# Kernel tuning notes

Measured on AMD Instinct MI355X. Metric: run time of the kernel, lower is better.

## Reference

```python
import jax, jax.numpy as jnp
import numpy as np

N = 100000   # nodes
E = 3200000  # edges
F = 128      # input features
H = 6        # hiddenSize
C = 10       # num_classes
G = 512      # graphs in batch


def setup_inputs() -> dict:
    key = jax.random.key(0)
    ks = jax.random.split(key, 13)
    x = jax.random.normal(ks[0], (N, F), dtype=jnp.float32)
    edge_index = jax.random.randint(ks[1], (2, E), 0, N, dtype=jnp.int32)
    batch = jnp.sort(jax.random.randint(ks[2], (N,), 0, G, dtype=jnp.int32))

    def lin(k, fan_in, fan_out):
        return jax.random.normal(k, (fan_in, fan_out), dtype=jnp.float32) / np.sqrt(fan_in).astype(np.float32)

    return {
        "x": x, "edge_index": edge_index, "batch": batch,
        "W1": lin(ks[3], F, H), "b1": jnp.zeros((H,), jnp.float32),
        "W2": lin(ks[4], H, H), "b2": jnp.zeros((H,), jnp.float32),
        "W3": lin(ks[5], H, H), "b3": jnp.zeros((H,), jnp.float32),
        "W4": lin(ks[6], H, H), "b4": jnp.zeros((H,), jnp.float32),
        "Wf": lin(ks[7], H, C), "bf": jnp.zeros((C,), jnp.float32),
    }


def _gcn_conv(x, W, b, src, dst, norm):
    # x' = scatter_add_{dst}( norm * (x W)[src] ) + b   (GCNConv, sym-norm, self-loops)
    h = x @ W
    msg = norm[:, None] * h[src]
    return jax.ops.segment_sum(msg, dst, num_segments=N) + b


def reference(x, edge_index, batch, W1, b1, W2, b2, W3, b3, W4, b4, Wf, bf):
    loops = jnp.arange(N, dtype=edge_index.dtype)
    src = jnp.concatenate([edge_index[0], loops])
    dst = jnp.concatenate([edge_index[1], loops])
    # degree (with self-loops) at the aggregation side, symmetric normalization
    deg = jax.ops.segment_sum(jnp.ones_like(dst, dtype=jnp.float32), dst, num_segments=N)
    dinv = jnp.where(deg > 0, jax.lax.rsqrt(deg), 0.0)
    norm = dinv[src] * dinv[dst]

    h = jax.nn.relu(_gcn_conv(x, W1, b1, src, dst, norm))
    h = jax.nn.relu(_gcn_conv(h, W2, b2, src, dst, norm))
    h = jax.nn.relu(_gcn_conv(h, W3, b3, src, dst, norm))
    h = jax.nn.relu(_gcn_conv(h, W4, b4, src, dst, norm))
    h = jax.nn.relu(_gcn_conv(h, Wf, bf, src, dst, norm))  # [N, C]

    # global_mean_pool over graph ids
    sums = jax.ops.segment_sum(h, batch, num_segments=G)          # [G, C]
    counts = jax.ops.segment_sum(jnp.ones((N,), jnp.float32), batch, num_segments=G)
    pooled = sums / jnp.maximum(counts, 1.0)[:, None]
    return jax.nn.log_softmax(pooled, axis=1)
```

## Files before the change

### kernel.cpp

```cpp
#include <hip/hip_runtime.h>
#include <math.h>

#define NN 100000
#define EE 3200000
#define FF 128
#define HH 6
#define CC 10
#define GG 512
#define NBUCK 196
#define BCAP 20000
#define NSUB 4
#define SUBCAP 5000
#define PTILE 16384
#define SUBIT 5
#define GWIN 16

typedef _Float16 half8 __attribute__((ext_vector_type(8)));

__global__ __launch_bounds__(256) void k_setup(const int* __restrict__ batch,
                                               int* __restrict__ gcur,
                                               int* __restrict__ bounds,
                                               float* __restrict__ gpool) {
    int i = blockIdx.x * 256 + threadIdx.x;
    if (i < NBUCK * NSUB) gcur[i] = (i >> 2) * BCAP + (i & 3) * SUBCAP;
    if (i <= GG) {
        int lo = 0, hi = NN;
        while (lo < hi) {
            int mid = (lo + hi) >> 1;
            if (batch[mid] < i) lo = mid + 1; else hi = mid;
        }
        bounds[i] = lo;
    }
    for (int j = i; j < GG * CC; j += 1024) gpool[j] = 0.f;
}

__global__ __launch_bounds__(1024) void k_partition(const int* __restrict__ src,
                                                    const int* __restrict__ dst,
                                                    int* __restrict__ gcur,
                                                    int* __restrict__ part) {
    __shared__ int lcnt[NBUCK], lbase[NBUCK];
    int t = threadIdx.x;
    int slot = blockIdx.x & (NSUB - 1);
    if (t < NBUCK) lcnt[t] = 0;
    __syncthreads();
    int base = blockIdx.x * PTILE;
    int d[16], s[16], r[16];
#pragma unroll
    for (int k = 0; k < 16; ++k) {
        int e = base + (k << 10) + t;
        d[k] = (e < EE) ? dst[e] : -1;
        s[k] = (e < EE) ? src[e] : 0;
    }
#pragma unroll
    for (int k = 0; k < 16; ++k)
        if (d[k] >= 0) r[k] = atomicAdd(&lcnt[d[k] >> 9], 1);
    __syncthreads();
    if (t < NBUCK) lbase[t] = lcnt[t] ? atomicAdd(&gcur[t * NSUB + slot], lcnt[t]) : 0;
    __syncthreads();
#pragma unroll
    for (int k = 0; k < 16; ++k) {
        if (d[k] >= 0) {
            int bkt = d[k] >> 9;
            part[lbase[bkt] + r[k]] = (s[k] << 9) | (d[k] & 511);
        }
    }
}

__global__ __launch_bounds__(1024) void k_bucketfill(const int* __restrict__ gcur,
                                                     const int* __restrict__ part,
                                                     int* __restrict__ csr,
                                                     int* __restrict__ rowptr,
                                                     int* __restrict__ counts,
                                                     float* __restrict__ dinv) {
    __shared__ int cnt[512];
    __shared__ int wsum[16];
    int t = threadIdx.x, b = blockIdx.x;
    int nbase = b << 9;
    int ebase = b * BCAP;
    int rend0 = gcur[b * NSUB + 0], rend1 = gcur[b * NSUB + 1];
    int rend2 = gcur[b * NSUB + 2], rend3 = gcur[b * NSUB + 3];
    if (t < 512) cnt[t] = 0;
    __syncthreads();
    int p[NSUB * SUBIT], r[NSUB * SUBIT];
#pragma unroll
    for (int q = 0; q < NSUB; ++q) {
        int rbase = ebase + q * SUBCAP;
        int rend = (q == 0) ? rend0 : (q == 1) ? rend1 : (q == 2) ? rend2 : rend3;
#pragma unroll
        for (int it = 0; it < SUBIT; ++it) {
            int j = rbase + (it << 10) + t;
            p[q * SUBIT + it] = (j < rend) ? part[j] : -1;
        }
    }
#pragma unroll
    for (int it = 0; it < NSUB * SUBIT; ++it)
        if (p[it] >= 0) r[it] = atomicAdd(&cnt[p[it] & 511], 1);
    __syncthreads();
    int c = (t < 512) ? cnt[t] : 0;
    int lane = t & 63, wv = t >> 6;
    int v = c;
#pragma unroll
    for (int off = 1; off < 64; off <<= 1) {
        int u = __shfl_up(v, off, 64);
        if (lane >= off) v += u;
    }
    if (lane == 63) wsum[wv] = v;
    __syncthreads();
    int acc = 0;
    for (int k = 0; k < wv; ++k) acc += wsum[k];
    int excl = ebase + acc + v - c;
    if (t < 512) {
        int node = nbase + t;
        if (node < NN) {
            rowptr[node] = excl;
            counts[node] = c;
            dinv[node] = rsqrtf((float)c + 1.0f);
        }
        cnt[t] = excl;
    }
    __syncthreads();
#pragma unroll
    for (int it = 0; it < NSUB * SUBIT; ++it)
        if (p[it] >= 0) csr[cnt[p[it] & 511] + r[it]] = p[it] >> 9;
}

__global__ __launch_bounds__(256) void k_xw1(const float* __restrict__ x,
                                             const float* __restrict__ W,
                                             const float* __restrict__ dinv,
                                             _Float16* __restrict__ hs) {
    __shared__ float sW[FF * HH];
    for (int i = threadIdx.x; i < FF * HH; i += 256) sW[i] = W[i];
    __syncthreads();
    int node = blockIdx.x * 64 + (threadIdx.x >> 2);
    int sub  = threadIdx.x & 3;
    if (node >= NN) return;
    const float4* xr = (const float4*)(x + (size_t)node * FF + sub * 32);
    float acc[HH];
#pragma unroll
    for (int c = 0; c < HH; ++c) acc[c] = 0.f;
#pragma unroll
    for (int q = 0; q < 8; ++q) {
        float4 v = xr[q];
        int k = sub * 32 + q * 4;
        const float* w0 = &sW[(k + 0) * HH];
        const float* w1 = &sW[(k + 1) * HH];
        const float* w2 = &sW[(k + 2) * HH];
        const float* w3 = &sW[(k + 3) * HH];
#pragma unroll
        for (int c = 0; c < HH; ++c)
            acc[c] += v.x * w0[c] + v.y * w1[c] + v.z * w2[c] + v.w * w3[c];
    }
#pragma unroll
    for (int c = 0; c < HH; ++c) {
        acc[c] += __shfl_xor(acc[c], 1, 64);
        acc[c] += __shfl_xor(acc[c], 2, 64);
    }
    if (sub == 0) {
        float di = dinv[node];
        half8 o;
#pragma unroll
        for (int c = 0; c < HH; ++c) o[c] = (_Float16)(di * acc[c]);
        o[6] = (_Float16)0.f; o[7] = (_Float16)0.f;
        *((half8*)(hs + (size_t)node * 8)) = o;
    }
}

template <int HON, int HPOH>
__global__ __launch_bounds__(256) void k_gf(const int* __restrict__ rowptr,
                                            const int* __restrict__ counts,
                                            const int* __restrict__ csr,
                                            const float* __restrict__ dinv,
                                            const _Float16* __restrict__ hs,
                                            const float* __restrict__ bias,
                                            const float* __restrict__ Wn,
                                            _Float16* __restrict__ outn) {
    __shared__ float sW[HH * HON];
    if (threadIdx.x < HH * HON) sW[threadIdx.x] = Wn[threadIdx.x];
    __syncthreads();
    int node = blockIdx.x * 64 + (threadIdx.x >> 2);
    int sub  = threadIdx.x & 3;
    if (node >= NN) return;
    int st = rowptr[node], cnt = counts[node];
    float a[HH];
    if (sub == 0) {
        half8 v = *((const half8*)(hs + (size_t)node * 8));
#pragma unroll
        for (int c = 0; c < HH; ++c) a[c] = (float)v[c];
    } else {
#pragma unroll
        for (int c = 0; c < HH; ++c) a[c] = 0.f;
    }
    int nfull = cnt >> 4;
#pragma unroll 2
    for (int m = 0; m < nfull; ++m) {
        int4 s4 = *((const int4*)(csr + st + (m << 4) + (sub << 2)));
        half8 v0 = *((const half8*)(hs + (size_t)s4.x * 8));
        half8 v1 = *((const half8*)(hs + (size_t)s4.y * 8));
        half8 v2 = *((const half8*)(hs + (size_t)s4.z * 8));
        half8 v3 = *((const half8*)(hs + (size_t)s4.w * 8));
#pragma unroll
        for (int c = 0; c < HH; ++c)
            a[c] += ((float)v0[c] + (float)v1[c]) + ((float)v2[c] + (float)v3[c]);
    }
    for (int j = st + (nfull << 4) + sub, end = st + cnt; j < end; j += 4) {
        int s = csr[j];
        half8 v = *((const half8*)(hs + (size_t)s * 8));
#pragma unroll
        for (int c = 0; c < HH; ++c) a[c] += (float)v[c];
    }
#pragma unroll
    for (int c = 0; c < HH; ++c) {
        a[c] += __shfl_xor(a[c], 1, 64);
        a[c] += __shfl_xor(a[c], 2, 64);
    }
    if (sub == 0) {
        float di = dinv[node];
        float h[HH];
#pragma unroll
        for (int c = 0; c < HH; ++c) h[c] = fmaxf(di * a[c] + bias[c], 0.f);
        half8 o[HPOH / 8];
#pragma unroll
        for (int c = 0; c < HPOH; ++c) {
            float s = 0.f;
            if (c < HON) {
#pragma unroll
                for (int k = 0; k < HH; ++k) s += h[k] * sW[k * HON + c];
                o[c / 8][c % 8] = (_Float16)(di * s);
            } else {
                o[c / 8][c % 8] = (_Float16)0.f;
            }
        }
        half8* op = (half8*)(outn + (size_t)node * HPOH);
#pragma unroll
        for (int q = 0; q < HPOH / 8; ++q) op[q] = o[q];
    }
}

__global__ __launch_bounds__(256) void k_glast(const int* __restrict__ rowptr,
                                               const int* __restrict__ counts,
                                               const int* __restrict__ csr,
                                               const float* __restrict__ dinv,
                                               const _Float16* __restrict__ hs,
                                               const float* __restrict__ bias,
                                               const int* __restrict__ batch,
                                               float* __restrict__ gpool) {
    __shared__ float gacc[GWIN * CC];
    int t = threadIdx.x;
    for (int i = t; i < GWIN * CC; i += 256) gacc[i] = 0.f;
    int node = blockIdx.x * 64 + (t >> 2);
    int sub  = t & 3;
    int gmin = batch[blockIdx.x * 64];
    __syncthreads();
    bool live = (node < NN);
    int st = 0, cnt = 0;
    if (live) { st = rowptr[node]; cnt = counts[node]; }
    float a[CC];
#pragma unroll
    for (int c = 0; c < CC; ++c) a[c] = 0.f;
    if (live && sub == 0) {
        const half8* p = (const half8*)(hs + (size_t)node * 16);
        half8 v0 = p[0], v1 = p[1];
#pragma unroll
        for (int c = 0; c < 8; ++c) a[c] = (float)v0[c];
        a[8] = (float)v1[0]; a[9] = (float)v1[1];
    }
    int nfull = cnt >> 4;
#pragma unroll 2
    for (int m = 0; m < nfull; ++m) {
        int4 s4 = *((const int4*)(csr + st + (m << 4) + (sub << 2)));
        const half8* p0 = (const half8*)(hs + (size_t)s4.x * 16);
        const half8* p1 = (const half8*)(hs + (size_t)s4.y * 16);
        const half8* p2 = (const half8*)(hs + (size_t)s4.z * 16);
        const half8* p3 = (const half8*)(hs + (size_t)s4.w * 16);
        half8 x0 = p0[0], y0 = p0[1], x1 = p1[0], y1 = p1[1];
        half8 x2 = p2[0], y2 = p2[1], x3 = p3[0], y3 = p3[1];
#pragma unroll
        for (int c = 0; c < 8; ++c)
            a[c] += ((float)x0[c] + (float)x1[c]) + ((float)x2[c] + (float)x3[c]);
        a[8] += ((float)y0[0] + (float)y1[0]) + ((float)y2[0] + (float)y3[0]);
        a[9] += ((float)y0[1] + (float)y1[1]) + ((float)y2[1] + (float)y3[1]);
    }
    for (int j = st + (nfull << 4) + sub, end = st + cnt; j < end; j += 4) {
        int s = csr[j];
        const half8* p = (const half8*)(hs + (size_t)s * 16);
        half8 x0 = p[0], y0 = p[1];
#pragma unroll
        for (int c = 0; c < 8; ++c) a[c] += (float)x0[c];
        a[8] += (float)y0[0]; a[9] += (float)y0[1];
    }
#pragma unroll
    for (int c = 0; c < CC; ++c) {
        a[c] += __shfl_xor(a[c], 1, 64);
        a[c] += __shfl_xor(a[c], 2, 64);
    }
    if (live && sub == 0) {
        float di = dinv[node];
        int g = batch[node];
        int off = g - gmin;
        if (off < GWIN) {
#pragma unroll
            for (int c = 0; c < CC; ++c) {
                float rv = fmaxf(di * a[c] + bias[c], 0.f);
                if (rv != 0.f) atomicAdd(&gacc[off * CC + c], rv);
            }
        } else {
#pragma unroll
            for (int c = 0; c < CC; ++c) {
                float rv = fmaxf(di * a[c] + bias[c], 0.f);
                if (rv != 0.f) atomicAdd(&gpool[(size_t)g * CC + c], rv);
            }
        }
    }
    __syncthreads();
    for (int i = t; i < GWIN * CC; i += 256) {
        float v = gacc[i];
        int g = gmin + i / CC;
        if (v != 0.f && g < GG) atomicAdd(&gpool[(size_t)g * CC + i % CC], v);
    }
}

__global__ __launch_bounds__(256) void k_poolfin(const float* __restrict__ gpool,
                                                 const int* __restrict__ bounds,
                                                 float* __restrict__ out) {
    int g = blockIdx.x * 256 + threadIdx.x;
    if (g >= GG) return;
    float cntf = fmaxf((float)(bounds[g + 1] - bounds[g]), 1.0f);
    float tot[CC];
    float m = -1e30f;
#pragma unroll
    for (int c = 0; c < CC; ++c) {
        tot[c] = gpool[(size_t)g * CC + c] / cntf;
        m = fmaxf(m, tot[c]);
    }
    float ss = 0.f;
#pragma unroll
    for (int c = 0; c < CC; ++c) ss += expf(tot[c] - m);
    float lse = logf(ss) + m;
#pragma unroll
    for (int c = 0; c < CC; ++c) out[(size_t)g * CC + c] = tot[c] - lse;
}

extern "C" void kernel_launch(void* const* d_in, const int* in_sizes, int n_in,
                              void* d_out, int out_size, void* d_ws, size_t ws_size,
                              hipStream_t stream) {
    const float* x     = (const float*)d_in[0];
    const int*   ei    = (const int*)d_in[1];
    const int*   batch = (const int*)d_in[2];
    const float* W1 = (const float*)d_in[3];
    const float* b1 = (const float*)d_in[4];
    const float* W2 = (const float*)d_in[5];
    const float* b2 = (const float*)d_in[6];
    const float* W3 = (const float*)d_in[7];
    const float* b3 = (const float*)d_in[8];
    const float* W4 = (const float*)d_in[9];
    const float* b4 = (const float*)d_in[10];
    const float* Wf = (const float*)d_in[11];
    const float* bf = (const float*)d_in[12];
    float* out = (float*)d_out;

    const int* src = ei;
    const int* dst = ei + EE;

    int*   iw     = (int*)d_ws;
    int*   csr    = iw;
    int*   rowptr = csr + 3920000;
    int*   counts = rowptr + 100352;
    float* dinv   = (float*)(counts + 100352);
    int*   gcur   = (int*)(dinv + 100352);
    int*   bounds = gcur + 1024;
    float* gpool  = (float*)(bounds + 640);
    int*   part   = (int*)(gpool + 5376);
    _Float16* hsA = (_Float16*)part;
    _Float16* hsB = hsA + 1605632;

    const int TB = (EE + PTILE - 1) / PTILE;
    const int GB = (NN + 63) / 64;

    k_setup<<<4, 256, 0, stream>>>(batch, gcur, bounds, gpool);
    k_partition<<<TB, 1024, 0, stream>>>(src, dst, gcur, part);
    k_bucketfill<<<NBUCK, 1024, 0, stream>>>(gcur, part, csr, rowptr, counts, dinv);

    k_xw1<<<GB, 256, 0, stream>>>(x, W1, dinv, hsA);
    k_gf<HH, 8><<<GB, 256, 0, stream>>>(rowptr, counts, csr, dinv, hsA, b1, W2, hsB);
    k_gf<HH, 8><<<GB, 256, 0, stream>>>(rowptr, counts, csr, dinv, hsB, b2, W3, hsA);
    k_gf<HH, 8><<<GB, 256, 0, stream>>>(rowptr, counts, csr, dinv, hsA, b3, W4, hsB);
    k_gf<CC, 16><<<GB, 256, 0, stream>>>(rowptr, counts, csr, dinv, hsB, b4, Wf, hsA);
    k_glast<<<GB, 256, 0, stream>>>(rowptr, counts, csr, dinv, hsA, bf, batch, gpool);

    k_poolfin<<<2, 256, 0, stream>>>(gpool, bounds, out);
}
```

Before: 198.2 us.

## Pad CSR rows to multiples of 16 with dummy zero node, drop gather tail loops

Each CSR row is padded to a multiple of 16 entries, with the padding pointing at a sentinel node index NN whose feature row is written as zeros in every layer's output buffer. The gather kernels can then drop their scalar remainder loop and run only the vectorized int4 main loop, with the unroll factor raised to 3. This removes divergent tail handling but adds up to 15 wasted gathers per node (an average degree of about 32 means roughly 20% extra gather traffic) and enlarges the CSR buffer.

```diff
diff --git a/kernel.cpp b/kernel.cpp
--- a/kernel.cpp
+++ b/kernel.cpp
@@ -9,6 +9,7 @@
 #define GG 512
 #define NBUCK 196
 #define BCAP 20000
+#define CCAP 21504
 #define NSUB 4
 #define SUBCAP 5000
 #define PTILE 16384
@@ -77,6 +78,7 @@
     int t = threadIdx.x, b = blockIdx.x;
     int nbase = b << 9;
     int ebase = b * BCAP;
+    int cbase = b * CCAP;
     int rend0 = gcur[b * NSUB + 0], rend1 = gcur[b * NSUB + 1];
     int rend2 = gcur[b * NSUB + 2], rend3 = gcur[b * NSUB + 3];
     if (t < 512) cnt[t] = 0;
@@ -97,8 +99,9 @@
         if (p[it] >= 0) r[it] = atomicAdd(&cnt[p[it] & 511], 1);
     __syncthreads();
     int c = (t < 512) ? cnt[t] : 0;
+    int pc = (c + 15) & ~15;
     int lane = t & 63, wv = t >> 6;
-    int v = c;
+    int v = pc;
 #pragma unroll
     for (int off = 1; off < 64; off <<= 1) {
         int u = __shfl_up(v, off, 64);
@@ -108,7 +111,7 @@
     __syncthreads();
     int acc = 0;
     for (int k = 0; k < wv; ++k) acc += wsum[k];
-    int excl = ebase + acc + v - c;
+    int excl = cbase + acc + v - pc;
     if (t < 512) {
         int node = nbase + t;
         if (node < NN) {
@@ -122,6 +125,9 @@
 #pragma unroll
     for (int it = 0; it < NSUB * SUBIT; ++it)
         if (p[it] >= 0) csr[cnt[p[it] & 511] + r[it]] = p[it] >> 9;
+    if (t < 512) {
+        for (int k = c; k < pc; ++k) csr[excl + k] = NN;
+    }
 }
 
 __global__ __launch_bounds__(256) void k_xw1(const float* __restrict__ x,
@@ -133,6 +139,12 @@
     __syncthreads();
     int node = blockIdx.x * 64 + (threadIdx.x >> 2);
     int sub  = threadIdx.x & 3;
+    if (blockIdx.x == 0 && threadIdx.x == 0) {
+        half8 z;
+#pragma unroll
+        for (int c = 0; c < 8; ++c) z[c] = (_Float16)0.f;
+        *((half8*)(hs + (size_t)NN * 8)) = z;
+    }
     if (node >= NN) return;
     const float4* xr = (const float4*)(x + (size_t)node * FF + sub * 32);
     float acc[HH];
@@ -179,6 +191,15 @@
     __syncthreads();
     int node = blockIdx.x * 64 + (threadIdx.x >> 2);
     int sub  = threadIdx.x & 3;
+    if (blockIdx.x == 0 && threadIdx.x == 0) {
+#pragma unroll
+        for (int q = 0; q < HPOH / 8; ++q) {
+            half8 z;
+#pragma unroll
+            for (int c = 0; c < 8; ++c) z[c] = (_Float16)0.f;
+            *((half8*)(outn + (size_t)NN * HPOH + q * 8)) = z;
+        }
+    }
     if (node >= NN) return;
     int st = rowptr[node], cnt = counts[node];
     float a[HH];
@@ -190,8 +211,8 @@
 #pragma unroll
         for (int c = 0; c < HH; ++c) a[c] = 0.f;
     }
-    int nfull = cnt >> 4;
-#pragma unroll 2
+    int nfull = ((cnt + 15) & ~15) >> 4;
+#pragma unroll 3
     for (int m = 0; m < nfull; ++m) {
         int4 s4 = *((const int4*)(csr + st + (m << 4) + (sub << 2)));
         half8 v0 = *((const half8*)(hs + (size_t)s4.x * 8));
@@ -201,12 +222,6 @@
 #pragma unroll
         for (int c = 0; c < HH; ++c)
             a[c] += ((float)v0[c] + (float)v1[c]) + ((float)v2[c] + (float)v3[c]);
-    }
-    for (int j = st + (nfull << 4) + sub, end = st + cnt; j < end; j += 4) {
-        int s = csr[j];
-        half8 v = *((const half8*)(hs + (size_t)s * 8));
-#pragma unroll
-        for (int c = 0; c < HH; ++c) a[c] += (float)v[c];
     }
 #pragma unroll
     for (int c = 0; c < HH; ++c) {
@@ -264,8 +279,8 @@
         for (int c = 0; c < 8; ++c) a[c] = (float)v0[c];
         a[8] = (float)v1[0]; a[9] = (float)v1[1];
     }
-    int nfull = cnt >> 4;
-#pragma unroll 2
+    int nfull = ((cnt + 15) & ~15) >> 4;
+#pragma unroll 3
     for (int m = 0; m < nfull; ++m) {
         int4 s4 = *((const int4*)(csr + st + (m << 4) + (sub << 2)));
         const half8* p0 = (const half8*)(hs + (size_t)s4.x * 16);
@@ -279,14 +294,6 @@
             a[c] += ((float)x0[c] + (float)x1[c]) + ((float)x2[c] + (float)x3[c]);
         a[8] += ((float)y0[0] + (float)y1[0]) + ((float)y2[0] + (float)y3[0]);
         a[9] += ((float)y0[1] + (float)y1[1]) + ((float)y2[1] + (float)y3[1]);
-    }
-    for (int j = st + (nfull << 4) + sub, end = st + cnt; j < end; j += 4) {
-        int s = csr[j];
-        const half8* p = (const half8*)(hs + (size_t)s * 16);
-        half8 x0 = p[0], y0 = p[1];
-#pragma unroll
-        for (int c = 0; c < 8; ++c) a[c] += (float)x0[c];
-        a[8] += (float)y0[0]; a[9] += (float)y0[1];
     }
 #pragma unroll
     for (int c = 0; c < CC; ++c) {
@@ -363,7 +370,7 @@
 
     int*   iw     = (int*)d_ws;
     int*   csr    = iw;
-    int*   rowptr = csr + 3920000;
+    int*   rowptr = csr + 4214784;
     int*   counts = rowptr + 100352;
     float* dinv   = (float*)(counts + 100352);
     int*   gcur   = (int*)(dinv + 100352);
```

Measured after the change: 195.0 us. About the same (-1.6%).
